# Performance work log

Measured on AMD Instinct MI355X. Metric: run time of the kernel, lower is better.

The kernel has to match this reference:

```python
import jax, jax.numpy as jnp
import numpy as np

NEG_SLOPE = 0.2
MASK_FILL = -9e10


def setup_inputs() -> dict:
    key = jax.random.key(0)
    ks = jax.random.split(key, 9)
    B, n_ope, n_mac = 32, 2048, 1024
    total = 64
    ope_dim, mac_dim, out_dim = 64, 64, 128
    ope_ma_adj = jax.random.randint(ks[0], (total, n_ope, n_mac), 0, 2, dtype=jnp.int32)
    batch_idxes = jax.random.randint(ks[1], (B,), 0, total, dtype=jnp.int64)
    feat_ope = jax.random.normal(ks[2], (B, n_ope, ope_dim), dtype=jnp.float32)
    feat_mac = jax.random.normal(ks[3], (B, n_mac, mac_dim), dtype=jnp.float32)
    # parameters (xavier-normal-like scaling)
    def xavier(k, shape):
        fan_in, fan_out = shape[1], shape[0]
        std = jnp.sqrt(2.0 / (fan_in + fan_out))
        return std * jax.random.normal(k, shape, dtype=jnp.float32)
    ope_w = xavier(ks[4], (out_dim, ope_dim))   # Linear weight [out, in]
    mac_w = xavier(ks[5], (out_dim, mac_dim))
    ope_alpha = xavier(ks[6], (out_dim, 1))
    mac_alpha = xavier(ks[7], (out_dim, 1))
    res_w = xavier(ks[8], (out_dim, mac_dim))
    return {
        "ope_ma_adj": ope_ma_adj, "batch_idxes": batch_idxes,
        "feat_ope": feat_ope, "feat_mac": feat_mac,
        "ope_w": ope_w, "mac_w": mac_w,
        "ope_alpha": ope_alpha, "mac_alpha": mac_alpha, "res_w": res_w,
    }


def reference(ope_ma_adj, batch_idxes, feat_ope, feat_mac,
              ope_w, mac_w, ope_alpha, mac_alpha, res_w):
    # dropout p=0 -> identity
    h_ope = jnp.einsum('bod,kd->bok', feat_ope, ope_w)   # [B, n_ope, out]
    h_mac = jnp.einsum('bmd,kd->bmk', feat_mac, mac_w)   # [B, n_mac, out]
    attn_ope = jnp.einsum('bok,k->bo', h_ope, ope_alpha[:, 0])  # [B, n_ope]
    attn_mac = jnp.einsum('bmk,k->bm', h_mac, mac_alpha[:, 0])  # [B, n_mac]
    e = attn_ope[:, :, None] + attn_mac[:, None, :]             # [B, n_ope, n_mac]
    e = jnp.where(e >= 0, e, NEG_SLOPE * e)                      # leaky relu
    mask = ope_ma_adj[batch_idxes] == 1                          # [B, n_ope, n_mac]
    e = jnp.where(mask, e, MASK_FILL)
    alpha = jax.nn.softmax(e, axis=-2)                           # over operations
    out = jnp.einsum('bom,bok->bmk', alpha, h_ope)               # [B, n_mac, out]
    h_res = jnp.einsum('bmd,kd->bmk', feat_mac, res_w)
    return out + h_res
```

## Files before the change

### kernel.cpp

```cpp
#include <hip/hip_runtime.h>

#define N_OPE 2048
#define N_MAC 1024
#define DIM   64
#define KOUT  128
#define NB    32

typedef __attribute__((ext_vector_type(8))) short short8;
typedef __attribute__((ext_vector_type(4))) float floatx4;

static __device__ __forceinline__ unsigned short f2bf(float f) {
    unsigned int u = __builtin_bit_cast(unsigned int, f);
    u += 0x7fffu + ((u >> 16) & 1u);
    return (unsigned short)(u >> 16);
}
static __device__ __forceinline__ float bf2f(unsigned short h) {
    unsigned int u = ((unsigned int)h) << 16;
    return __builtin_bit_cast(float, u);
}

__global__ __launch_bounds__(256, 2) void k_ope(const float* __restrict__ feat,
        const float* __restrict__ w, const float* __restrict__ alpha,
        unsigned short* __restrict__ h_f, float2* __restrict__ pq)
{
    int wid = threadIdx.x >> 6, lane = threadIdx.x & 63;
    int L = lane & 15, q = lane >> 4;
    int base = blockIdx.x * 128 + wid * 32;
    int b = base >> 11;
    int o0w = base & (N_OPE - 1);

    float fA[2][2][8];
    #pragma unroll
    for (int mf = 0; mf < 2; ++mf) {
        const float* fr = feat + (size_t)(base + mf * 16 + L) * DIM + q * 8;
        #pragma unroll
        for (int ks = 0; ks < 2; ++ks) {
            float4 v0 = *(const float4*)(fr + ks * 32);
            float4 v1 = *(const float4*)(fr + ks * 32 + 4);
            fA[mf][ks][0] = v0.x; fA[mf][ks][1] = v0.y; fA[mf][ks][2] = v0.z; fA[mf][ks][3] = v0.w;
            fA[mf][ks][4] = v1.x; fA[mf][ks][5] = v1.y; fA[mf][ks][6] = v1.z; fA[mf][ks][7] = v1.w;
        }
    }

    short8 Ah[2][2], Al[2][2];
    #pragma unroll
    for (int mf = 0; mf < 2; ++mf)
        #pragma unroll
        for (int ks = 0; ks < 2; ++ks)
            #pragma unroll
            for (int j = 0; j < 8; ++j) {
                float x = fA[mf][ks][j];
                unsigned short h = f2bf(x);
                Ah[mf][ks][j] = (short)h;
                Al[mf][ks][j] = (short)f2bf(x - bf2f(h));
            }

    floatx4 C[2][8];
    #pragma unroll
    for (int mf = 0; mf < 2; ++mf)
        #pragma unroll
        for (int nf = 0; nf < 8; ++nf) C[mf][nf] = (floatx4)0.f;

    #pragma unroll
    for (int ks = 0; ks < 2; ++ks) {
        #pragma unroll
        for (int nf = 0; nf < 8; ++nf) {
            const float* wp = w + (size_t)(nf * 16 + L) * DIM + ks * 32 + q * 8;
            float4 u0 = *(const float4*)(wp);
            float4 u1 = *(const float4*)(wp + 4);
            float bw[8] = {u0.x, u0.y, u0.z, u0.w, u1.x, u1.y, u1.z, u1.w};
            short8 Bh, Bl;
            #pragma unroll
            for (int j = 0; j < 8; ++j) {
                unsigned short h = f2bf(bw[j]);
                Bh[j] = (short)h;
                Bl[j] = (short)f2bf(bw[j] - bf2f(h));
            }
            #pragma unroll
            for (int mf = 0; mf < 2; ++mf) {
                C[mf][nf] = __builtin_amdgcn_mfma_f32_16x16x32_bf16(Ah[mf][ks], Bh, C[mf][nf], 0, 0, 0);
                C[mf][nf] = __builtin_amdgcn_mfma_f32_16x16x32_bf16(Al[mf][ks], Bh, C[mf][nf], 0, 0, 0);
                C[mf][nf] = __builtin_amdgcn_mfma_f32_16x16x32_bf16(Ah[mf][ks], Bl, C[mf][nf], 0, 0, 0);
            }
        }
    }

    float alf[8];
    #pragma unroll
    for (int nf = 0; nf < 8; ++nf) alf[nf] = alpha[nf * 16 + L];
    #pragma unroll
    for (int mf = 0; mf < 2; ++mf) {
        #pragma unroll
        for (int r = 0; r < 4; ++r) {
            float s = 0.f;
            #pragma unroll
            for (int nf = 0; nf < 8; ++nf) s = fmaf(C[mf][nf][r], alf[nf], s);
            s += __shfl_xor(s, 1); s += __shfl_xor(s, 2);
            s += __shfl_xor(s, 4); s += __shfl_xor(s, 8);
            if (L == 0)
                pq[base + mf * 16 + q * 4 + r] = make_float2(__expf(s), __expf(0.2f * s));
        }
    }

    __shared__ unsigned short T[4][128 * 40];
    #pragma unroll
    for (int mf = 0; mf < 2; ++mf)
        #pragma unroll
        for (int nf = 0; nf < 8; ++nf)
            #pragma unroll
            for (int r = 0; r < 4; ++r)
                T[wid][(nf * 16 + L) * 40 + mf * 16 + q * 4 + r] = f2bf(C[mf][nf][r]);
    __syncthreads();

    int oc = o0w >> 5;
    unsigned short* dst = h_f + ((((size_t)b * 64 + oc) * 8) * 64 + lane) * 8;
    #pragma unroll
    for (int nf = 0; nf < 8; ++nf) {
        short8 v = *(const short8*)&T[wid][(nf * 16 + L) * 40 + q * 8];
        *(short8*)(dst + (size_t)nf * 512) = v;
    }
}

__global__ __launch_bounds__(256) void k_attn(const int* __restrict__ adj,
        const int* __restrict__ bidx,
        const unsigned short* __restrict__ h_f,
        const float2* __restrict__ pq,
        const float* __restrict__ feat_mac,
        const float* __restrict__ mac_w, const float* __restrict__ mac_alpha,
        const float* __restrict__ res_w,
        float* __restrict__ out)
{
    int b  = blockIdx.y;
    int m0 = blockIdx.x * 32;
    int t = threadIdx.x, wv = t >> 6, lane = t & 63;
    int L = lane & 15, q = lane >> 4;

    __shared__ float buf0[32 * 132];
    __shared__ float buf1[32 * 132];
    __shared__ float waS[64];
    __shared__ float amS[32];
    __shared__ float DS[4][32];

    {
        int d = t & 63, seg = t >> 6;
        float p = 0.f;
        #pragma unroll 8
        for (int n = seg * 32; n < seg * 32 + 32; ++n)
            p = fmaf(mac_w[n * DIM + d], mac_alpha[n], p);
        buf0[seg * 64 + d] = p;
    }
    __syncthreads();
    if (t < 64) waS[t] = buf0[t] + buf0[64 + t] + buf0[128 + t] + buf0[192 + t];
    __syncthreads();
    {
        int row = t & 31, seg = t >> 5;
        const float* fr = feat_mac + ((size_t)b * N_MAC + m0 + row) * DIM + seg * 8;
        float p = 0.f;
        #pragma unroll
        for (int k = 0; k < 8; ++k) p = fmaf(fr[k], waS[seg * 8 + k], p);
        buf1[seg * 32 + row] = p;
    }
    __syncthreads();
    if (t < 32) {
        float s = 0.f;
        #pragma unroll
        for (int sg = 0; sg < 8; ++sg) s += buf1[sg * 32 + t];
        amS[t] = s;
    }
    __syncthreads();

    float2 amv = *(const float2*)&amS[2 * L];
    float pM0 = __expf(amv.x), qM0 = __expf(0.2f * amv.x);
    float pM1 = __expf(amv.y), qM1 = __expf(0.2f * amv.y);

    const int* adjt = adj + (size_t)bidx[b] * (N_OPE * N_MAC);
    const unsigned short* hfb = h_f + (size_t)b * (64 * 8 * 64 * 8);
    const float2* pqb = pq + (size_t)b * N_OPE;

    floatx4 C0[8], C1[8];
    #pragma unroll
    for (int i = 0; i < 8; ++i) { C0[i] = (floatx4)0.f; C1[i] = (floatx4)0.f; }
    float den0 = 0.f, den1 = 0.f;

    int oBeg = wv * (N_OPE / 4);
    for (int o0 = oBeg; o0 < oBeg + N_OPE / 4; o0 += 32) {
        int ob = o0 + q * 8;
        float4 pv0 = *(const float4*)(pqb + ob);
        float4 pv1 = *(const float4*)(pqb + ob + 2);
        float4 pv2 = *(const float4*)(pqb + ob + 4);
        float4 pv3 = *(const float4*)(pqb + ob + 6);
        float pA[8] = {pv0.x, pv0.z, pv1.x, pv1.z, pv2.x, pv2.z, pv3.x, pv3.z};
        float qA[8] = {pv0.y, pv0.w, pv1.y, pv1.w, pv2.y, pv2.w, pv3.y, pv3.w};

        int2 mk[8];
        #pragma unroll
        for (int j = 0; j < 8; ++j)
            mk[j] = *(const int2*)(adjt + (size_t)(ob + j) * N_MAC + m0 + 2 * L);

        const unsigned short* fp = hfb + (((size_t)(o0 >> 5) * 8) * 64 + lane) * 8;
        short8 Bf[8];
        #pragma unroll
        for (int nf = 0; nf < 8; ++nf)
            Bf[nf] = *(const short8*)(fp + (size_t)nf * 512);

        float w0v[8], w1v[8];
        #pragma unroll
        for (int j = 0; j < 8; ++j) {
            float tp0 = pA[j] * pM0;
            float w0 = (tp0 >= 1.0f) ? tp0 : qA[j] * qM0;
            w0 = (mk[j].x == 1) ? w0 : 0.f;
            den0 += w0; w0v[j] = w0;
            float tp1 = pA[j] * pM1;
            float w1 = (tp1 >= 1.0f) ? tp1 : qA[j] * qM1;
            w1 = (mk[j].y == 1) ? w1 : 0.f;
            den1 += w1; w1v[j] = w1;
        }
        int4 A0i, A1i;
        #pragma unroll
        for (int j2 = 0; j2 < 4; ++j2) {
            unsigned lo0 = __builtin_bit_cast(unsigned, w0v[2 * j2])     + 0x8000u;
            unsigned hi0 = __builtin_bit_cast(unsigned, w0v[2 * j2 + 1]) + 0x8000u;
            ((unsigned*)&A0i)[j2] = __builtin_amdgcn_perm(hi0, lo0, 0x07060302u);
            unsigned lo1 = __builtin_bit_cast(unsigned, w1v[2 * j2])     + 0x8000u;
            unsigned hi1 = __builtin_bit_cast(unsigned, w1v[2 * j2 + 1]) + 0x8000u;
            ((unsigned*)&A1i)[j2] = __builtin_amdgcn_perm(hi1, lo1, 0x07060302u);
        }
        short8 A0 = __builtin_bit_cast(short8, A0i);
        short8 A1 = __builtin_bit_cast(short8, A1i);

        #pragma unroll
        for (int nf = 0; nf < 8; ++nf) {
            C0[nf] = __builtin_amdgcn_mfma_f32_16x16x32_bf16(A0, Bf[nf], C0[nf], 0, 0, 0);
            C1[nf] = __builtin_amdgcn_mfma_f32_16x16x32_bf16(A1, Bf[nf], C1[nf], 0, 0, 0);
        }
    }

    den0 += __shfl_xor(den0, 16); den0 += __shfl_xor(den0, 32);
    den1 += __shfl_xor(den1, 16); den1 += __shfl_xor(den1, 32);
    if (q == 0) { DS[wv][L] = den0; DS[wv][16 + L] = den1; }

    if (wv == 0 || wv == 2) {
        float* bp = (wv == 0) ? buf0 : buf1;
        #pragma unroll
        for (int mf = 0; mf < 2; ++mf) {
            const floatx4* Cf = mf ? C1 : C0;
            #pragma unroll
            for (int nf = 0; nf < 8; ++nf)
                #pragma unroll
                for (int r = 0; r < 4; ++r)
                    bp[(mf * 16 + q * 4 + r) * 132 + nf * 16 + L] = Cf[nf][r];
        }
    }
    __syncthreads();
    if (wv == 1 || wv == 3) {
        float* bp = (wv == 1) ? buf0 : buf1;
        #pragma unroll
        for (int mf = 0; mf < 2; ++mf) {
            const floatx4* Cf = mf ? C1 : C0;
            #pragma unroll
            for (int nf = 0; nf < 8; ++nf)
                #pragma unroll
                for (int r = 0; r < 4; ++r)
                    bp[(mf * 16 + q * 4 + r) * 132 + nf * 16 + L] += Cf[nf][r];
        }
    }
    __syncthreads();

    float fA[2][2][8];
    #pragma unroll
    for (int mf = 0; mf < 2; ++mf) {
        const float* fr = feat_mac + ((size_t)b * N_MAC + m0 + 2 * L + mf) * DIM + q * 8;
        #pragma unroll
        for (int ks = 0; ks < 2; ++ks) {
            float4 v0 = *(const float4*)(fr + ks * 32);
            float4 v1 = *(const float4*)(fr + ks * 32 + 4);
            fA[mf][ks][0] = v0.x; fA[mf][ks][1] = v0.y; fA[mf][ks][2] = v0.z; fA[mf][ks][3] = v0.w;
            fA[mf][ks][4] = v1.x; fA[mf][ks][5] = v1.y; fA[mf][ks][6] = v1.z; fA[mf][ks][7] = v1.w;
        }
    }
    short8 Ah[2][2], Al[2][2];
    #pragma unroll
    for (int mf = 0; mf < 2; ++mf)
        #pragma unroll
        for (int ks = 0; ks < 2; ++ks)
            #pragma unroll
            for (int j = 0; j < 8; ++j) {
                float x = fA[mf][ks][j];
                unsigned short h = f2bf(x);
                Ah[mf][ks][j] = (short)h;
                Al[mf][ks][j] = (short)f2bf(x - bf2f(h));
            }
    floatx4 R[2][2];
    R[0][0] = (floatx4)0.f; R[0][1] = (floatx4)0.f;
    R[1][0] = (floatx4)0.f; R[1][1] = (floatx4)0.f;
    #pragma unroll
    for (int ks = 0; ks < 2; ++ks) {
        #pragma unroll
        for (int nfl = 0; nfl < 2; ++nfl) {
            const float* wp = res_w + (size_t)((wv * 2 + nfl) * 16 + L) * DIM + ks * 32 + q * 8;
            float4 u0 = *(const float4*)(wp);
            float4 u1 = *(const float4*)(wp + 4);
            float bw[8] = {u0.x, u0.y, u0.z, u0.w, u1.x, u1.y, u1.z, u1.w};
            short8 Bh, Bl;
            #pragma unroll
            for (int j = 0; j < 8; ++j) {
                unsigned short h = f2bf(bw[j]);
                Bh[j] = (short)h;
                Bl[j] = (short)f2bf(bw[j] - bf2f(h));
            }
            #pragma unroll
            for (int mf = 0; mf < 2; ++mf) {
                R[mf][nfl] = __builtin_amdgcn_mfma_f32_16x16x32_bf16(Ah[mf][ks], Bh, R[mf][nfl], 0, 0, 0);
                R[mf][nfl] = __builtin_amdgcn_mfma_f32_16x16x32_bf16(Al[mf][ks], Bh, R[mf][nfl], 0, 0, 0);
                R[mf][nfl] = __builtin_amdgcn_mfma_f32_16x16x32_bf16(Ah[mf][ks], Bl, R[mf][nfl], 0, 0, 0);
            }
        }
    }

    #pragma unroll
    for (int mf = 0; mf < 2; ++mf) {
        #pragma unroll
        for (int r = 0; r < 4; ++r) {
            int fragrow = q * 4 + r;
            int m = m0 + 2 * fragrow + mf;
            float inv = 1.0f / (DS[0][mf * 16 + fragrow] + DS[1][mf * 16 + fragrow]
                              + DS[2][mf * 16 + fragrow] + DS[3][mf * 16 + fragrow]);
            size_t obase = ((size_t)b * N_MAC + m) * KOUT;
            #pragma unroll
            for (int nfl = 0; nfl < 2; ++nfl) {
                int col = (wv * 2 + nfl) * 16 + L;
                float num = buf0[(mf * 16 + fragrow) * 132 + col]
                          + buf1[(mf * 16 + fragrow) * 132 + col];
                out[obase + col] = num * inv + R[mf][nfl][r];
            }
        }
    }
}

extern "C" void kernel_launch(void* const* d_in, const int* in_sizes, int n_in,
                              void* d_out, int out_size, void* d_ws, size_t ws_size,
                              hipStream_t stream) {
    const int*   adj       = (const int*)d_in[0];
    const int*   bidx      = (const int*)d_in[1];
    const float* feat_ope  = (const float*)d_in[2];
    const float* feat_mac  = (const float*)d_in[3];
    const float* ope_w     = (const float*)d_in[4];
    const float* mac_w     = (const float*)d_in[5];
    const float* ope_alpha = (const float*)d_in[6];
    const float* mac_alpha = (const float*)d_in[7];
    const float* res_w     = (const float*)d_in[8];
    float* out = (float*)d_out;

    char* ws = (char*)d_ws;
    unsigned short* h_f = (unsigned short*)ws;
    float2* pq          = (float2*)(ws + (size_t)(16 << 20));

    k_ope<<<512, 256, 0, stream>>>(feat_ope, ope_w, ope_alpha, h_f, pq);
    k_attn<<<dim3(N_MAC / 32, NB), 256, 0, stream>>>(adj, bidx, h_f, pq, feat_mac,
                                                     mac_w, mac_alpha, res_w, out);
}
```

Before: 695.0 us.

## Pre-pack adjacency mask to bits and precompute mac attention terms

Adds a pre-pass kernel that compresses the int32 adjacency rows for each batch into a bitmask laid out per 32-machine chunk. The attention kernel then reads one packed word per operation instead of strided int2 loads. The per-machine attention exponentials move into a separate small kernel, and the attention grid is reindexed so batches sharing L2 are interleaved. The full int32 adjacency is still read once in the pack pass, and the change adds two extra launches plus workspace traffic.

```diff
diff --git a/kernel.cpp b/kernel.cpp
--- a/kernel.cpp
+++ b/kernel.cpp
@@ -17,6 +17,41 @@
 static __device__ __forceinline__ float bf2f(unsigned short h) {
     unsigned int u = ((unsigned int)h) << 16;
     return __builtin_bit_cast(float, u);
+}
+
+__global__ __launch_bounds__(256) void k_pack(const int* __restrict__ adj,
+        const int* __restrict__ bidx, unsigned* __restrict__ pk)
+{
+    __shared__ unsigned P[32][65];
+    int bid = blockIdx.x;
+    int b = bid >> 5, obase = (bid & 31) * 64;
+    int t = threadIdx.x;
+    const int* adjr = adj + (size_t)bidx[b] * (N_OPE * N_MAC) + (size_t)obase * N_MAC;
+
+    #pragma unroll
+    for (int w = 0; w < 8; ++w) {
+        int idx = w * 256 + t;
+        int r = idx >> 5, mc = idx & 31;
+        const int4* p = (const int4*)(adjr + r * N_MAC + mc * 32);
+        unsigned word = 0;
+        #pragma unroll
+        for (int k = 0; k < 8; ++k) {
+            int4 v = p[k];
+            word |= (unsigned)(v.x & 1) << (4 * k);
+            word |= (unsigned)(v.y & 1) << (4 * k + 1);
+            word |= (unsigned)(v.z & 1) << (4 * k + 2);
+            word |= (unsigned)(v.w & 1) << (4 * k + 3);
+        }
+        P[mc][r] = word;
+    }
+    __syncthreads();
+    unsigned* dst = pk + ((size_t)b * 32) * N_OPE + obase;
+    int oi = t & 63;
+    #pragma unroll
+    for (int ww = 0; ww < 8; ++ww) {
+        int mc = ww * 4 + (t >> 6);
+        dst[(size_t)mc * N_OPE + oi] = P[mc][oi];
+    }
 }
 
 __global__ __launch_bounds__(256, 2) void k_ope(const float* __restrict__ feat,
@@ -121,61 +156,54 @@
     }
 }
 
-__global__ __launch_bounds__(256) void k_attn(const int* __restrict__ adj,
-        const int* __restrict__ bidx,
-        const unsigned short* __restrict__ h_f,
-        const float2* __restrict__ pq,
-        const float* __restrict__ feat_mac,
+__global__ __launch_bounds__(256) void k_amac(const float* __restrict__ feat_mac,
         const float* __restrict__ mac_w, const float* __restrict__ mac_alpha,
-        const float* __restrict__ res_w,
-        float* __restrict__ out)
+        float2* __restrict__ pqM)
 {
-    int b  = blockIdx.y;
-    int m0 = blockIdx.x * 32;
-    int t = threadIdx.x, wv = t >> 6, lane = t & 63;
-    int L = lane & 15, q = lane >> 4;
-
-    __shared__ float buf0[32 * 132];
-    __shared__ float buf1[32 * 132];
+    __shared__ float partial[256];
     __shared__ float waS[64];
-    __shared__ float amS[32];
-    __shared__ float DS[4][32];
-
+    int t = threadIdx.x;
     {
         int d = t & 63, seg = t >> 6;
         float p = 0.f;
         #pragma unroll 8
         for (int n = seg * 32; n < seg * 32 + 32; ++n)
             p = fmaf(mac_w[n * DIM + d], mac_alpha[n], p);
-        buf0[seg * 64 + d] = p;
-    }
-    __syncthreads();
-    if (t < 64) waS[t] = buf0[t] + buf0[64 + t] + buf0[128 + t] + buf0[192 + t];
-    __syncthreads();
-    {
-        int row = t & 31, seg = t >> 5;
-        const float* fr = feat_mac + ((size_t)b * N_MAC + m0 + row) * DIM + seg * 8;
-        float p = 0.f;
-        #pragma unroll
-        for (int k = 0; k < 8; ++k) p = fmaf(fr[k], waS[seg * 8 + k], p);
-        buf1[seg * 32 + row] = p;
-    }
-    __syncthreads();
-    if (t < 32) {
-        float s = 0.f;
-        #pragma unroll
-        for (int sg = 0; sg < 8; ++sg) s += buf1[sg * 32 + t];
-        amS[t] = s;
-    }
-    __syncthreads();
-
-    float2 amv = *(const float2*)&amS[2 * L];
-    float pM0 = __expf(amv.x), qM0 = __expf(0.2f * amv.x);
-    float pM1 = __expf(amv.y), qM1 = __expf(0.2f * amv.y);
-
-    const int* adjt = adj + (size_t)bidx[b] * (N_OPE * N_MAC);
+        partial[seg * 64 + d] = p;
+    }
+    __syncthreads();
+    if (t < 64) waS[t] = partial[t] + partial[64 + t] + partial[128 + t] + partial[192 + t];
+    __syncthreads();
+    int row = blockIdx.x * 256 + t;
+    const float* fr = feat_mac + (size_t)row * DIM;
+    float s = 0.f;
+    #pragma unroll
+    for (int k = 0; k < DIM; k += 4) {
+        float4 v = *(const float4*)(fr + k);
+        s = fmaf(v.x, waS[k], s); s = fmaf(v.y, waS[k + 1], s);
+        s = fmaf(v.z, waS[k + 2], s); s = fmaf(v.w, waS[k + 3], s);
+    }
+    pqM[row] = make_float2(__expf(s), __expf(0.2f * s));
+}
+
+__global__ __launch_bounds__(256) void k_attn(const unsigned* __restrict__ pk,
+        const unsigned short* __restrict__ h_f,
+        const float2* __restrict__ pq, const float2* __restrict__ pqM,
+        const float* __restrict__ feat_mac, const float* __restrict__ res_w,
+        float* __restrict__ out)
+{
+    int lin = blockIdx.x;
+    int b   = 4 * (lin & 7) + ((lin >> 3) & 3);
+    int m0  = (lin >> 5) * 32;
+    int t = threadIdx.x, wv = t >> 6, lane = t & 63;
+    int L = lane & 15, q = lane >> 4;
+
+    const unsigned* pkb = pk + ((size_t)b * 32 + (m0 >> 5)) * N_OPE;
     const unsigned short* hfb = h_f + (size_t)b * (64 * 8 * 64 * 8);
     const float2* pqb = pq + (size_t)b * N_OPE;
+
+    float4 pm = *(const float4*)(pqM + (size_t)b * N_MAC + m0 + 2 * L);
+    float pM0 = pm.x, qM0 = pm.y, pM1 = pm.z, qM1 = pm.w;
 
     floatx4 C0[8], C1[8];
     #pragma unroll
@@ -192,10 +220,9 @@
         float pA[8] = {pv0.x, pv0.z, pv1.x, pv1.z, pv2.x, pv2.z, pv3.x, pv3.z};
         float qA[8] = {pv0.y, pv0.w, pv1.y, pv1.w, pv2.y, pv2.w, pv3.y, pv3.w};
 
-        int2 mk[8];
-        #pragma unroll
-        for (int j = 0; j < 8; ++j)
-            mk[j] = *(const int2*)(adjt + (size_t)(ob + j) * N_MAC + m0 + 2 * L);
+        uint4 wk0 = *(const uint4*)(pkb + ob);
+        uint4 wk1 = *(const uint4*)(pkb + ob + 4);
+        unsigned wkv[8] = {wk0.x, wk0.y, wk0.z, wk0.w, wk1.x, wk1.y, wk1.z, wk1.w};
 
         const unsigned short* fp = hfb + (((size_t)(o0 >> 5) * 8) * 64 + lane) * 8;
         short8 Bf[8];
@@ -206,13 +233,14 @@
         float w0v[8], w1v[8];
         #pragma unroll
         for (int j = 0; j < 8; ++j) {
+            unsigned bits = wkv[j] >> (2 * L);
             float tp0 = pA[j] * pM0;
             float w0 = (tp0 >= 1.0f) ? tp0 : qA[j] * qM0;
-            w0 = (mk[j].x == 1) ? w0 : 0.f;
+            w0 = (bits & 1u) ? w0 : 0.f;
             den0 += w0; w0v[j] = w0;
             float tp1 = pA[j] * pM1;
             float w1 = (tp1 >= 1.0f) ? tp1 : qA[j] * qM1;
-            w1 = (mk[j].y == 1) ? w1 : 0.f;
+            w1 = (bits & 2u) ? w1 : 0.f;
             den1 += w1; w1v[j] = w1;
         }
         int4 A0i, A1i;
@@ -237,6 +265,10 @@
 
     den0 += __shfl_xor(den0, 16); den0 += __shfl_xor(den0, 32);
     den1 += __shfl_xor(den1, 16); den1 += __shfl_xor(den1, 32);
+
+    __shared__ float buf0[32 * 132];
+    __shared__ float buf1[32 * 132];
+    __shared__ float DS[4][32];
     if (q == 0) { DS[wv][L] = den0; DS[wv][16 + L] = den1; }
 
     if (wv == 0 || wv == 2) {
@@ -354,8 +386,11 @@
     char* ws = (char*)d_ws;
     unsigned short* h_f = (unsigned short*)ws;
     float2* pq          = (float2*)(ws + (size_t)(16 << 20));
-
+    float2* pqM         = (float2*)(ws + (size_t)(16 << 20) + (512 << 10));
+    unsigned* pk        = (unsigned*)(ws + (size_t)(17 << 20));
+
+    k_pack<<<1024, 256, 0, stream>>>(adj, bidx, pk);
     k_ope<<<512, 256, 0, stream>>>(feat_ope, ope_w, ope_alpha, h_f, pq);
-    k_attn<<<dim3(N_MAC / 32, NB), 256, 0, stream>>>(adj, bidx, h_f, pq, feat_mac,
-                                                     mac_w, mac_alpha, res_w, out);
-}
+    k_amac<<<128, 256, 0, stream>>>(feat_mac, mac_w, mac_alpha, pqM);
+    k_attn<<<1024, 256, 0, stream>>>(pk, h_f, pq, pqM, feat_mac, res_w, out);
+}
```

After: 730.8 us. 5.2% more time.
